# Kernel optimization log

Hardware: AMD Instinct MI355X
Metric: run time of the kernel (lower is better)

## Reference

```python
import jax, jax.numpy as jnp
import numpy as np

DIM = 768
NUM_HEADS = 12
HEAD_DIM = DIM // NUM_HEADS


def setup_inputs() -> dict:
    key = jax.random.key(0)
    k1, k2, k3 = jax.random.split(key, 3)
    B, N, C = 8, 4096, DIM
    x = jax.random.normal(k1, (B, N, C), dtype=jnp.float32)
    # torch nn.Linear weights are (out_features, in_features)
    W_qkv = jax.random.normal(k2, (3 * C, C), dtype=jnp.float32) * 0.02
    b_qkv = jnp.zeros((3 * C,), dtype=jnp.float32)
    W_proj = jax.random.normal(k3, (C, C), dtype=jnp.float32) * 0.02
    b_proj = jnp.zeros((C,), dtype=jnp.float32)
    return {"x": x, "W_qkv": W_qkv, "b_qkv": b_qkv, "W_proj": W_proj, "b_proj": b_proj}


def reference(x, W_qkv, b_qkv, W_proj, b_proj):
    B, N, C = x.shape
    H, D = NUM_HEADS, HEAD_DIM
    # qkv projection -> (3, B, H, N, D)
    qkv = (x @ W_qkv.T + b_qkv).reshape(B, N, 3, H, D).transpose(2, 0, 3, 1, 4)
    q, k, v = qkv[0], qkv[1], qkv[2]
    # feature map: elu(x) + 1 (positive kernel features)
    q = jax.nn.elu(q) + 1.0
    k = jax.nn.elu(k) + 1.0
    # kernelized linear attention: (K^T V) then Q (K^T V)
    kv = jnp.einsum('bhnd,bhnv->bhdv', k, v)          # (B,H,D,D)
    out = jnp.einsum('bhnd,bhdv->bhnv', q, kv)        # (B,H,N,D)
    k_sum = k.sum(axis=2)                             # (B,H,D)
    normalizer = jnp.einsum('bhnd,bhd->bhn', q, k_sum) + 1e-06
    out = out / normalizer[..., None]
    out = out.transpose(0, 2, 1, 3).reshape(B, N, C)
    out = out @ W_proj.T + b_proj
    return out
```

## Files before the change

### kernel.cpp

```cpp
#include <hip/hip_runtime.h>
#include <hip/hip_fp16.h>
#include <math.h>

#define NHEADS 12
#define SEQ 4096
#define BATCH 8

typedef _Float16 half8 __attribute__((ext_vector_type(8)));
typedef float floatx4 __attribute__((ext_vector_type(4)));

__global__ void zero_kernel(float* p, int n) {
  int i = blockIdx.x * 256 + threadIdx.x;
  if (i < n) p[i] = 0.f;
}

__global__ void cast_f2h(const float* __restrict__ in, __half* __restrict__ out, int n) {
  int i = (blockIdx.x * 256 + threadIdx.x) * 4;
  if (i < n) {
    float4 v = *(const float4*)&in[i];
    ushort4 o;
    o.x = __half_as_ushort(__float2half(v.x));
    o.y = __half_as_ushort(__float2half(v.y));
    o.z = __half_as_ushort(__float2half(v.z));
    o.w = __half_as_ushort(__float2half(v.w));
    *(ushort4*)&out[i] = o;
  }
}

__device__ __forceinline__ void gld16(const __half* g, _Float16* dst) {
  __builtin_amdgcn_global_load_lds((const __attribute__((address_space(1))) void*)g,
                                   (__attribute__((address_space(3))) void*)dst, 16, 0, 0);
}

__device__ __forceinline__ int fragoff(int row, int quad) {
  const int mp = row >> 1;
  const int p  = ((row & 1) << 2) | quad;
  return (mp * 8 + (p ^ (mp & 7))) * 8;
}

__device__ __forceinline__ void stage_tile(const __half* __restrict__ gbase, int ldg,
                                           _Float16* lds, int t) {
#pragma unroll
  for (int it = 0; it < 2; ++it) {
    const int s  = it * 256 + t;
    const int mp = s >> 3, ps = s & 7;
    const int p  = ps ^ (mp & 7);
    const int r  = mp * 2 + (p >> 2);
    const int q  = p & 3;
    const __half* g = gbase + (size_t)r * ldg + q * 8;
    _Float16* dst = lds + (s >> 6) * 512;
    gld16(g, dst);
  }
}

__device__ __forceinline__ void write_l64(_Float16* lds, int row, int col, float v) {
  lds[row * 64 + ((((col >> 3) ^ (row & 7))) << 3) + (col & 7)] = (_Float16)v;
}
__device__ __forceinline__ half8 read_l64c(const _Float16* lds, int row, int c) {
  return *(const half8*)(lds + row * 64 + ((c ^ (row & 7)) << 3));
}

__device__ __forceinline__ void barrier_raw() {
  asm volatile("s_barrier" ::: "memory");
}

__global__ __launch_bounds__(512, 2) void hgemm_kv8_kernel(
    const __half* __restrict__ A, const __half* __restrict__ W,
    const float* __restrict__ bias,
    __half* __restrict__ outK, __half* __restrict__ outV)
{
  const int K = 768;
  const int NT = 24;
  extern __shared__ __align__(16) _Float16 sh[];
  const int t    = threadIdx.x;
  const int w    = t >> 6;
  const int l    = t & 63;
  const int quad = l >> 4;
  const int mrow = l & 15;
  const int wm   = w >> 2;
  const int wn   = w & 3;

  const int bid  = blockIdx.x;
  const int xcd  = bid & 7;
  const int ii   = bid >> 3;
  const int mg   = ii / 6;
  const int jj   = ii - mg * 6;
  const int m0   = (xcd * 16 + mg) * 256;
  const int j0   = jj * 256;

  const int mp  = t >> 3;
  const int pp  = (t & 7) ^ (mp & 7);
  const int rsw = mp * 2 + (pp >> 2);
  const int qsw = (pp & 3) * 8;
  const __half* gA0 = A + (size_t)(m0 + rsw) * K + qsw;
  const __half* gA1 = gA0 + (size_t)128 * K;
  const __half* gW0 = W + (size_t)(768 + j0 + rsw) * K + qsw;
  const __half* gW1 = gW0 + (size_t)128 * K;
  const int ld = (t >> 6) * 512;

  int aoff[8], boff[4];
#pragma unroll
  for (int i = 0; i < 8; ++i)
    aoff[i] = wm * 4096 + fragoff(i * 16 + mrow, quad);
#pragma unroll
  for (int j = 0; j < 4; ++j) {
    const int C = wn * 64 + j * 16 + mrow;
    boff[j] = 8192 + (C >> 7) * 4096 + fragoff(C & 127, quad);
  }

  floatx4 acc[8][4];
#pragma unroll
  for (int i = 0; i < 8; ++i)
#pragma unroll
    for (int j = 0; j < 4; ++j) acc[i][j] = (floatx4){0.f, 0.f, 0.f, 0.f};

#pragma unroll
  for (int kt = 0; kt < 3; ++kt) {
    _Float16* db = sh + kt * 16384;
    const int kg = kt * 32;
    gld16(gA0 + kg, db + ld);
    gld16(gA1 + kg, db + 4096 + ld);
    gld16(gW0 + kg, db + 8192 + ld);
    gld16(gW1 + kg, db + 12288 + ld);
  }
  asm volatile("s_waitcnt vmcnt(8)" ::: "memory");
  barrier_raw();

#pragma unroll 4
  for (int kt = 0; kt < NT; ++kt) {
    const _Float16* bb = sh + (kt & 3) * 16384;
    const bool st = (kt + 3 < NT);
    _Float16* db = sh + ((kt + 3) & 3) * 16384;
    const int kg = (kt + 3) * 32;
    half8 af[4], bf[4];

#pragma unroll
    for (int j = 0; j < 4; ++j) bf[j] = *(const half8*)(bb + boff[j]);
#pragma unroll
    for (int i = 0; i < 4; ++i) af[i] = *(const half8*)(bb + aoff[i]);
    if (st) {
      gld16(gA0 + kg, db + ld);
      gld16(gA1 + kg, db + 4096 + ld);
    }
    barrier_raw();
    __builtin_amdgcn_s_setprio(1);
#pragma unroll
    for (int i = 0; i < 4; ++i)
#pragma unroll
      for (int j = 0; j < 4; ++j)
        acc[i][j] = __builtin_amdgcn_mfma_f32_16x16x32_f16(af[i], bf[j], acc[i][j], 0, 0, 0);
    __builtin_amdgcn_s_setprio(0);

#pragma unroll
    for (int i = 0; i < 4; ++i) af[i] = *(const half8*)(bb + aoff[i + 4]);
    if (st) {
      gld16(gW0 + kg, db + 8192 + ld);
      gld16(gW1 + kg, db + 12288 + ld);
    }
    barrier_raw();
    __builtin_amdgcn_s_setprio(1);
#pragma unroll
    for (int i = 0; i < 4; ++i)
#pragma unroll
      for (int j = 0; j < 4; ++j)
        acc[i + 4][j] = __builtin_amdgcn_mfma_f32_16x16x32_f16(af[i], bf[j], acc[i + 4][j], 0, 0, 0);
    __builtin_amdgcn_s_setprio(0);

    if (kt < NT - 3)       asm volatile("s_waitcnt vmcnt(8)" ::: "memory");
    else if (kt == NT - 3) asm volatile("s_waitcnt vmcnt(4)" ::: "memory");
    else if (kt == NT - 2) asm volatile("s_waitcnt vmcnt(0)" ::: "memory");
    barrier_raw();
  }

  const int col0 = 768 + j0 + wn * 64;
  const int t3   = col0 / 768;
  const int h    = (col0 - t3 * 768) >> 6;
  __half* dst    = (t3 == 1) ? outK : outV;
  const int m0w  = m0 + wm * 128;
  const int b_   = m0w >> 12;
  const int n0w  = m0w & 4095;
  _Float16* scr  = sh + w * 4096;
  const size_t gbT = (size_t)(b_ * NHEADS + h) * 64 * 4096;

#pragma unroll
  for (int hf = 0; hf < 2; ++hf) {
#pragma unroll
    for (int j = 0; j < 4; ++j) {
      const int col = j * 16 + mrow;
      const float bsv = bias[col0 + col];
#pragma unroll
      for (int ii2 = 0; ii2 < 4; ++ii2)
#pragma unroll
        for (int r = 0; r < 4; ++r) {
          const int row = ii2 * 16 + quad * 4 + r;
          float val = acc[hf * 4 + ii2][j][r] + bsv;
          if (t3 == 1) val = (val > 0.f) ? (val + 1.f) : expf(val);
          write_l64(scr, col, row, val);
        }
    }
    barrier_raw();
#pragma unroll
    for (int it = 0; it < 8; ++it) {
      const int dd = it * 8 + (l >> 3);
      const int c  = l & 7;
      half8 vv = read_l64c(scr, dd, c);
      *(half8*)((_Float16*)dst + gbT + (size_t)dd * 4096 + n0w + hf * 64 + c * 8) = vv;
    }
    barrier_raw();
  }
}

__global__ __launch_bounds__(256, 3) void hgemm_proj_kernel(
    const __half* __restrict__ A, const __half* __restrict__ W,
    const float* __restrict__ bias, float* __restrict__ outF)
{
  const int K = 768;
  const int NT = 24;
  __shared__ __align__(16) _Float16 sh[3 * 8192];
  const int t    = threadIdx.x;
  const int w    = t >> 6;
  const int l    = t & 63;
  const int quad = l >> 4;
  const int mrow = l & 15;
  const int wr   = (w >> 1) * 64;
  const int wc   = (w & 1) * 64;

  const int bid  = blockIdx.x;
  const int xcd  = bid & 7;
  const int ii   = bid >> 3;
  const int mg   = ii / 6;
  const int jj   = ii - mg * 6;
  const int m0   = (xcd * 32 + mg) * 128;
  const int j0   = jj * 128;

  const int s1  = 256 + t;
  const int mpa = t >> 3,  ppa = (t & 7) ^ (mpa & 7);
  const int ra  = mpa * 2 + (ppa >> 2), qa = (ppa & 3) * 8;
  const int mpb = s1 >> 3, ppb = (s1 & 7) ^ (mpb & 7);
  const int rb  = mpb * 2 + (ppb >> 2), qb = (ppb & 3) * 8;
  const int lda_ = (t >> 6) * 512;
  const int ldb_ = (s1 >> 6) * 512;
  const __half* gA_0 = A + (size_t)(m0 + ra) * K + qa;
  const __half* gA_1 = A + (size_t)(m0 + rb) * K + qb;
  const __half* gB_0 = W + (size_t)(j0 + ra) * K + qa;
  const __half* gB_1 = W + (size_t)(j0 + rb) * K + qb;

  int aoff[4], boff[4];
#pragma unroll
  for (int i = 0; i < 4; ++i) aoff[i] = fragoff(wr + i * 16 + mrow, quad);
#pragma unroll
  for (int j = 0; j < 4; ++j) boff[j] = 4096 + fragoff(wc + j * 16 + mrow, quad);

  floatx4 acc[4][4];
#pragma unroll
  for (int i = 0; i < 4; ++i)
#pragma unroll
    for (int j = 0; j < 4; ++j) acc[i][j] = (floatx4){0.f, 0.f, 0.f, 0.f};

  gld16(gA_0, sh + lda_);           gld16(gA_1, sh + ldb_);
  gld16(gB_0, sh + 4096 + lda_);    gld16(gB_1, sh + 4096 + ldb_);
  gld16(gA_0 + 32, sh + 8192 + lda_);        gld16(gA_1 + 32, sh + 8192 + ldb_);
  gld16(gB_0 + 32, sh + 12288 + lda_);       gld16(gB_1 + 32, sh + 12288 + ldb_);
  asm volatile("s_waitcnt vmcnt(4)" ::: "memory");
  barrier_raw();

  int cur = 0, nxt = 2;
#pragma unroll 3
  for (int kt = 0; kt < NT; ++kt) {
    const _Float16* bb = sh + cur * 8192;
    _Float16* db = sh + nxt * 8192;
    const bool st = (kt + 2 < NT);
    const int kg = (kt + 2) * 32;

    if (st) {
      gld16(gA_0 + kg, db + lda_);        gld16(gA_1 + kg, db + ldb_);
      gld16(gB_0 + kg, db + 4096 + lda_); gld16(gB_1 + kg, db + 4096 + ldb_);
    }
    half8 af[4], bf[4];
#pragma unroll
    for (int i = 0; i < 4; ++i) af[i] = *(const half8*)(bb + aoff[i]);
#pragma unroll
    for (int j = 0; j < 4; ++j) bf[j] = *(const half8*)(bb + boff[j]);
#pragma unroll
    for (int i = 0; i < 4; ++i)
#pragma unroll
      for (int j = 0; j < 4; ++j)
        acc[i][j] = __builtin_amdgcn_mfma_f32_16x16x32_f16(af[i], bf[j], acc[i][j], 0, 0, 0);

    if (kt < NT - 2)       asm volatile("s_waitcnt vmcnt(4)" ::: "memory");
    else if (kt == NT - 2) asm volatile("s_waitcnt vmcnt(0)" ::: "memory");
    barrier_raw();
    cur = (cur + 1) % 3;
    nxt = (nxt + 1) % 3;
  }

#pragma unroll
  for (int j = 0; j < 4; ++j) {
    const int col = j0 + wc + j * 16 + mrow;
    const float bsv = bias[col];
#pragma unroll
    for (int i = 0; i < 4; ++i)
#pragma unroll
      for (int r = 0; r < 4; ++r) {
        const int m = m0 + wr + i * 16 + quad * 4 + r;
        outF[(size_t)m * 768 + col] = acc[i][j][r] + bsv;
      }
  }
}

__global__ __launch_bounds__(256) void kv_mfma_kernel(
    const __half* __restrict__ kT, const __half* __restrict__ vT,
    float* __restrict__ kv, float* __restrict__ ksum)
{
  extern __shared__ float red[];
  float* ksr = red + 4 * 4096;
  const int bh = blockIdx.x;
  const int sp = blockIdx.y;
  const int t  = threadIdx.x;
  const int w  = t >> 6;
  const int l  = t & 63;
  const int quad = l >> 4;
  const int mrow = l & 15;
  const size_t base = (size_t)bh * 64 * 4096;
  const int n0 = sp * 1024 + w * 256;

  floatx4 acc[4][4];
  floatx4 ks[4];
#pragma unroll
  for (int i = 0; i < 4; ++i) {
    ks[i] = (floatx4){0.f, 0.f, 0.f, 0.f};
#pragma unroll
    for (int j = 0; j < 4; ++j) acc[i][j] = (floatx4){0.f, 0.f, 0.f, 0.f};
  }
  half8 ones;
#pragma unroll
  for (int e = 0; e < 8; ++e) ones[e] = (_Float16)1.0f;

  const __half* pk[4];
  const __half* pv[4];
#pragma unroll
  for (int i = 0; i < 4; ++i) {
    pk[i] = kT + base + (size_t)(i * 16 + mrow) * 4096 + n0 + quad * 8;
    pv[i] = vT + base + (size_t)(i * 16 + mrow) * 4096 + n0 + quad * 8;
  }

#pragma unroll
  for (int nn = 0; nn < 256; nn += 32) {
    half8 af[4], bf[4];
#pragma unroll
    for (int i = 0; i < 4; ++i) af[i] = *(const half8*)(pk[i] + nn);
#pragma unroll
    for (int j = 0; j < 4; ++j) bf[j] = *(const half8*)(pv[j] + nn);
#pragma unroll
    for (int i = 0; i < 4; ++i)
#pragma unroll
      for (int j = 0; j < 4; ++j)
        acc[i][j] = __builtin_amdgcn_mfma_f32_16x16x32_f16(af[i], bf[j], acc[i][j], 0, 0, 0);
#pragma unroll
    for (int i = 0; i < 4; ++i)
      ks[i] = __builtin_amdgcn_mfma_f32_16x16x32_f16(af[i], ones, ks[i], 0, 0, 0);
  }

  float* rw = red + w * 4096;
#pragma unroll
  for (int i = 0; i < 4; ++i)
#pragma unroll
    for (int j = 0; j < 4; ++j)
#pragma unroll
      for (int r = 0; r < 4; ++r)
        rw[(i * 16 + quad * 4 + r) * 64 + j * 16 + mrow] = acc[i][j][r];
  if (mrow == 0) {
#pragma unroll
    for (int i = 0; i < 4; ++i)
#pragma unroll
      for (int r = 0; r < 4; ++r)
        ksr[w * 64 + i * 16 + quad * 4 + r] = ks[i][r];
  }
  __syncthreads();
#pragma unroll
  for (int ii = 0; ii < 16; ++ii) {
    const int idx = ii * 256 + t;
    const float s = red[idx] + red[4096 + idx] + red[8192 + idx] + red[12288 + idx];
    atomicAdd(&kv[(size_t)bh * 4096 + idx], s);
  }
  if (t < 64)
    atomicAdd(&ksum[(size_t)bh * 64 + t], ksr[t] + ksr[64 + t] + ksr[128 + t] + ksr[192 + t]);
}

__global__ __launch_bounds__(512, 2) void qattn_kernel(
    const __half* __restrict__ A, const __half* __restrict__ W,
    const float* __restrict__ bias,
    const float* __restrict__ kvg, const float* __restrict__ ksumg,
    __half* __restrict__ att)
{
  const int K = 768;
  const int NT = 24;
  extern __shared__ __align__(16) _Float16 sh[];
  __shared__ float norms[512];
  __shared__ float ksums[128];
  const int t    = threadIdx.x;
  const int w    = t >> 6;
  const int l    = t & 63;
  const int quad = l >> 4;
  const int mrow = l & 15;
  const int wr   = (w >> 1) * 64;
  const int hh   = w & 1;
  const int wc   = hh * 64;

  const int bid = blockIdx.x;
  const int xcd = bid & 7;
  const int ii  = bid >> 3;
  const int mg  = ii / 6;
  const int jj  = ii - mg * 6;
  const int m0  = (xcd * 16 + mg) * 256;
  const int j0  = jj * 128;
  const int b_  = m0 >> 12;
  const int h0  = jj * 2;

  _Float16* kvT0 = sh + 49152;

#pragma unroll
  for (int it = 0; it < 16; ++it) {
    const int gidx = it * 512 + t;
    const int head = gidx >> 12;
    const int r    = gidx & 4095;
    const float val = kvg[(size_t)(b_ * NHEADS + h0 + head) * 4096 + r];
    write_l64(kvT0 + head * 4096, r & 63, r >> 6, val);
  }
  if (t < 128) ksums[t] = ksumg[(size_t)(b_ * NHEADS + h0 + (t >> 6)) * 64 + (t & 63)];

  const int mp  = t >> 3;
  const int pp  = (t & 7) ^ (mp & 7);
  const int rsw = mp * 2 + (pp >> 2);
  const int qsw = (pp & 3) * 8;
  const __half* gA0 = A + (size_t)(m0 + rsw) * K + qsw;
  const __half* gA1 = gA0 + (size_t)128 * K;
  const __half* gB0 = W + (size_t)(j0 + rsw) * K + qsw;
  const int ld = (t >> 6) * 512;

  int aoff[4], boff[4];
#pragma unroll
  for (int i = 0; i < 4; ++i) {
    const int rowi = wr + i * 16 + mrow;
    aoff[i] = (rowi >> 7) * 4096 + fragoff(rowi & 127, quad);
  }
#pragma unroll
  for (int j = 0; j < 4; ++j) boff[j] = 8192 + fragoff(wc + j * 16 + mrow, quad);

  floatx4 acc[4][4];
#pragma unroll
  for (int i = 0; i < 4; ++i)
#pragma unroll
    for (int j = 0; j < 4; ++j) acc[i][j] = (floatx4){0.f, 0.f, 0.f, 0.f};

#pragma unroll
  for (int kt = 0; kt < 3; ++kt) {
    _Float16* db = sh + kt * 12288;
    const int kg = kt * 32;
    gld16(gA0 + kg, db + ld);
    gld16(gA1 + kg, db + 4096 + ld);
    gld16(gB0 + kg, db + 8192 + ld);
  }
  asm volatile("s_waitcnt vmcnt(6)" ::: "memory");
  barrier_raw();

#pragma unroll 4
  for (int kt = 0; kt < NT; ++kt) {
    const _Float16* bb = sh + (kt & 3) * 12288;
    const bool st = (kt + 3 < NT);
    _Float16* db = sh + ((kt + 3) & 3) * 12288;
    const int kg = (kt + 3) * 32;
    half8 af[4], bf[4];

#pragma unroll
    for (int j = 0; j < 4; ++j) bf[j] = *(const half8*)(bb + boff[j]);
#pragma unroll
    for (int i = 0; i < 4; ++i) af[i] = *(const half8*)(bb + aoff[i]);
    if (st) {
      gld16(gA0 + kg, db + ld);
      gld16(gA1 + kg, db + 4096 + ld);
      gld16(gB0 + kg, db + 8192 + ld);
    }
#pragma unroll
    for (int i = 0; i < 4; ++i)
#pragma unroll
      for (int j = 0; j < 4; ++j)
        acc[i][j] = __builtin_amdgcn_mfma_f32_16x16x32_f16(af[i], bf[j], acc[i][j], 0, 0, 0);

    if (kt < NT - 3)       asm volatile("s_waitcnt vmcnt(6)" ::: "memory");
    else if (kt == NT - 3) asm volatile("s_waitcnt vmcnt(3)" ::: "memory");
    else if (kt == NT - 2) asm volatile("s_waitcnt vmcnt(0)" ::: "memory");
    barrier_raw();
  }

  _Float16* qtile = sh + w * 4096;

#pragma unroll
  for (int j = 0; j < 4; ++j) {
    const int col = j * 16 + mrow;
    const float bsv = bias[j0 + wc + col];
#pragma unroll
    for (int i = 0; i < 4; ++i)
#pragma unroll
      for (int r = 0; r < 4; ++r) {
        const int row = i * 16 + quad * 4 + r;
        float val = acc[i][j][r] + bsv;
        val = (val > 0.f) ? (val + 1.f) : expf(val);
        write_l64(qtile, row, col, val);
      }
  }
  asm volatile("s_waitcnt lgkmcnt(0)" ::: "memory");
  __builtin_amdgcn_sched_barrier(0);

  {
    float nrm = 0.f;
#pragma unroll
    for (int c = 0; c < 8; ++c) {
      half8 qv = read_l64c(qtile, l, c);
#pragma unroll
      for (int e = 0; e < 8; ++e) nrm += (float)qv[e] * ksums[hh * 64 + c * 8 + e];
    }
    norms[w * 64 + l] = 1.f / (nrm + 1e-6f);
  }

  const _Float16* kvT = kvT0 + hh * 4096;
  floatx4 oacc[4][4];
#pragma unroll
  for (int i = 0; i < 4; ++i)
#pragma unroll
    for (int j = 0; j < 4; ++j) oacc[i][j] = (floatx4){0.f, 0.f, 0.f, 0.f};
#pragma unroll
  for (int ks = 0; ks < 2; ++ks) {
    half8 af2[4], bf2[4];
#pragma unroll
    for (int i = 0; i < 4; ++i) af2[i] = read_l64c(qtile, i * 16 + mrow, ks * 4 + quad);
#pragma unroll
    for (int j = 0; j < 4; ++j) bf2[j] = read_l64c(kvT, j * 16 + mrow, ks * 4 + quad);
#pragma unroll
    for (int i = 0; i < 4; ++i)
#pragma unroll
      for (int j = 0; j < 4; ++j)
        oacc[i][j] = __builtin_amdgcn_mfma_f32_16x16x32_f16(af2[i], bf2[j], oacc[i][j], 0, 0, 0);
  }
  asm volatile("s_waitcnt lgkmcnt(0)" ::: "memory");
  __builtin_amdgcn_sched_barrier(0);

#pragma unroll
  for (int i = 0; i < 4; ++i)
#pragma unroll
    for (int r = 0; r < 4; ++r) {
      const int row = i * 16 + quad * 4 + r;
      const float rn = norms[w * 64 + row];
#pragma unroll
      for (int j = 0; j < 4; ++j)
        write_l64(qtile, row, j * 16 + mrow, oacc[i][j][r] * rn);
    }
  asm volatile("s_waitcnt lgkmcnt(0)" ::: "memory");
  __builtin_amdgcn_sched_barrier(0);

  const int n0w = (m0 & 4095) + wr;
  const size_t abase = (size_t)(b_ * SEQ + n0w) * 768 + (h0 + hh) * 64;
#pragma unroll
  for (int it = 0; it < 8; ++it) {
    const int row = it * 8 + (l >> 3);
    const int c   = l & 7;
    half8 vv = read_l64c(qtile, row, c);
    *(half8*)((_Float16*)att + abase + (size_t)row * 768 + c * 8) = vv;
  }
}

extern "C" void kernel_launch(void* const* d_in, const int* in_sizes, int n_in,
                              void* d_out, int out_size, void* d_ws, size_t ws_size,
                              hipStream_t stream)
{
  const float* x     = (const float*)d_in[0];
  const float* Wqkv  = (const float*)d_in[1];
  const float* bqkv  = (const float*)d_in[2];
  const float* Wproj = (const float*)d_in[3];
  const float* bproj = (const float*)d_in[4];
  float* out = (float*)d_out;

  const size_t SZ = (size_t)BATCH * NHEADS * SEQ * 64;
  __half* xh  = (__half*)d_ws;
  __half* Wqh = xh + SZ;
  __half* Wph = Wqh + (size_t)2304 * 768;
  __half* R3  = Wph + (size_t)768 * 768;
  __half* R4  = R3 + SZ;
  float*  kvb = (float*)(R4 + SZ);
  float*  ksum = kvb + 96 * 64 * 64;

  static bool attr_set = false;
  if (!attr_set) {
    hipFuncSetAttribute((const void*)hgemm_kv8_kernel,
                        hipFuncAttributeMaxDynamicSharedMemorySize, 131072);
    hipFuncSetAttribute((const void*)kv_mfma_kernel,
                        hipFuncAttributeMaxDynamicSharedMemorySize, 66560);
    hipFuncSetAttribute((const void*)qattn_kernel,
                        hipFuncAttributeMaxDynamicSharedMemorySize, 114688);
    attr_set = true;
  }

  zero_kernel<<<1560, 256, 0, stream>>>(kvb, 96 * 64 * 64 + 96 * 64);

  cast_f2h<<<(int)(SZ / 1024), 256, 0, stream>>>(x, xh, (int)SZ);
  cast_f2h<<<(2304 * 768) / 1024, 256, 0, stream>>>(Wqkv, Wqh, 2304 * 768);
  cast_f2h<<<(768 * 768) / 1024, 256, 0, stream>>>(Wproj, Wph, 768 * 768);

  hgemm_kv8_kernel<<<768, 512, 131072, stream>>>(xh, Wqh, bqkv, R3, R4);

  kv_mfma_kernel<<<dim3(96, 4), 256, 66560, stream>>>(R3, R4, kvb, ksum);

  qattn_kernel<<<768, 512, 114688, stream>>>(
      xh, Wqh, bqkv, kvb, ksum, R3);

  hgemm_proj_kernel<<<1536, 256, 0, stream>>>(R3, Wph, bproj, out);
}
```

Baseline: 442.6 us.

## Restructure KV GEMM pipeline into double-buffered 64-wide K stages

Replaces the 4-deep ring of 32-wide K tiles in the K/V projection GEMM with a double buffer of 64-wide K stages (two 32-wide sub-tiles each), so the loop runs 12 iterations instead of 24. Waits and barriers are placed at sub-tile boundaries, with prefetch of the next stage interleaved between MFMA groups. The aim is to cut per-iteration loop and barrier overhead while keeping loads in flight. In exchange it adds extra barriers per sub-tile and has a shallower prefetch distance, which may expose memory latency. It also removes an unused staging helper.

```diff
diff --git a/kernel.cpp b/kernel.cpp
--- a/kernel.cpp
+++ b/kernel.cpp
@@ -38,21 +38,6 @@
   return (mp * 8 + (p ^ (mp & 7))) * 8;
 }
 
-__device__ __forceinline__ void stage_tile(const __half* __restrict__ gbase, int ldg,
-                                           _Float16* lds, int t) {
-#pragma unroll
-  for (int it = 0; it < 2; ++it) {
-    const int s  = it * 256 + t;
-    const int mp = s >> 3, ps = s & 7;
-    const int p  = ps ^ (mp & 7);
-    const int r  = mp * 2 + (p >> 2);
-    const int q  = p & 3;
-    const __half* g = gbase + (size_t)r * ldg + q * 8;
-    _Float16* dst = lds + (s >> 6) * 512;
-    gld16(g, dst);
-  }
-}
-
 __device__ __forceinline__ void write_l64(_Float16* lds, int row, int col, float v) {
   lds[row * 64 + ((((col >> 3) ^ (row & 7))) << 3) + (col & 7)] = (_Float16)v;
 }
@@ -70,7 +55,7 @@
     __half* __restrict__ outK, __half* __restrict__ outV)
 {
   const int K = 768;
-  const int NT = 24;
+  const int NKT = 12;
   extern __shared__ __align__(16) _Float16 sh[];
   const int t    = threadIdx.x;
   const int w    = t >> 6;
@@ -98,50 +83,51 @@
   const __half* gW1 = gW0 + (size_t)128 * K;
   const int ld = (t >> 6) * 512;
 
-  int aoff[8], boff[4];
+  int aoff0[8], aoff1[8], boff0[4], boff1[4];
+#pragma unroll
+  for (int i = 0; i < 8; ++i) {
+    const int fo = fragoff(i * 16 + mrow, quad);
+    aoff0[i] = wm * 4096 + fo;
+    aoff1[i] = (2 + wm) * 4096 + fo;
+  }
+#pragma unroll
+  for (int j = 0; j < 4; ++j) {
+    const int C  = wn * 64 + j * 16 + mrow;
+    const int fo = fragoff(C & 127, quad);
+    boff0[j] = 16384 + (C >> 7) * 4096 + fo;
+    boff1[j] = 16384 + (2 + (C >> 7)) * 4096 + fo;
+  }
+
+  floatx4 acc[8][4];
 #pragma unroll
   for (int i = 0; i < 8; ++i)
-    aoff[i] = wm * 4096 + fragoff(i * 16 + mrow, quad);
-#pragma unroll
-  for (int j = 0; j < 4; ++j) {
-    const int C = wn * 64 + j * 16 + mrow;
-    boff[j] = 8192 + (C >> 7) * 4096 + fragoff(C & 127, quad);
-  }
-
-  floatx4 acc[8][4];
-#pragma unroll
-  for (int i = 0; i < 8; ++i)
 #pragma unroll
     for (int j = 0; j < 4; ++j) acc[i][j] = (floatx4){0.f, 0.f, 0.f, 0.f};
 
-#pragma unroll
-  for (int kt = 0; kt < 3; ++kt) {
-    _Float16* db = sh + kt * 16384;
-    const int kg = kt * 32;
-    gld16(gA0 + kg, db + ld);
-    gld16(gA1 + kg, db + 4096 + ld);
-    gld16(gW0 + kg, db + 8192 + ld);
-    gld16(gW1 + kg, db + 12288 + ld);
-  }
-  asm volatile("s_waitcnt vmcnt(8)" ::: "memory");
-  barrier_raw();
-
-#pragma unroll 4
-  for (int kt = 0; kt < NT; ++kt) {
-    const _Float16* bb = sh + (kt & 3) * 16384;
-    const bool st = (kt + 3 < NT);
-    _Float16* db = sh + ((kt + 3) & 3) * 16384;
-    const int kg = (kt + 3) * 32;
+  gld16(gA0,      sh + ld);
+  gld16(gA1,      sh + 4096  + ld);
+  gld16(gW0,      sh + 16384 + ld);
+  gld16(gW1,      sh + 20480 + ld);
+  gld16(gA0 + 32, sh + 8192  + ld);
+  gld16(gA1 + 32, sh + 12288 + ld);
+  gld16(gW0 + 32, sh + 24576 + ld);
+  gld16(gW1 + 32, sh + 28672 + ld);
+
+#pragma unroll 2
+  for (int kt = 0; kt < NKT; ++kt) {
+    const _Float16* bb = sh + (kt & 1) * 32768;
+    _Float16* db = sh + ((kt + 1) & 1) * 32768;
+    const bool st = (kt + 1 < NKT);
+    const int kg = (kt + 1) * 64;
     half8 af[4], bf[4];
 
-#pragma unroll
-    for (int j = 0; j < 4; ++j) bf[j] = *(const half8*)(bb + boff[j]);
-#pragma unroll
-    for (int i = 0; i < 4; ++i) af[i] = *(const half8*)(bb + aoff[i]);
-    if (st) {
-      gld16(gA0 + kg, db + ld);
-      gld16(gA1 + kg, db + 4096 + ld);
-    }
+    asm volatile("s_waitcnt vmcnt(4)" ::: "memory");
+    barrier_raw();
+#pragma unroll
+    for (int j = 0; j < 4; ++j) bf[j] = *(const half8*)(bb + boff0[j]);
+#pragma unroll
+    for (int i = 0; i < 4; ++i) af[i] = *(const half8*)(bb + aoff0[i]);
+    if (st) { gld16(gA0 + kg, db + ld); gld16(gA1 + kg, db + 4096 + ld); }
     barrier_raw();
     __builtin_amdgcn_s_setprio(1);
 #pragma unroll
@@ -151,12 +137,10 @@
         acc[i][j] = __builtin_amdgcn_mfma_f32_16x16x32_f16(af[i], bf[j], acc[i][j], 0, 0, 0);
     __builtin_amdgcn_s_setprio(0);
 
-#pragma unroll
-    for (int i = 0; i < 4; ++i) af[i] = *(const half8*)(bb + aoff[i + 4]);
-    if (st) {
-      gld16(gW0 + kg, db + 8192 + ld);
-      gld16(gW1 + kg, db + 12288 + ld);
-    }
+    barrier_raw();
+#pragma unroll
+    for (int i = 0; i < 4; ++i) af[i] = *(const half8*)(bb + aoff0[i + 4]);
+    if (st) { gld16(gW0 + kg, db + 16384 + ld); gld16(gW1 + kg, db + 20480 + ld); }
     barrier_raw();
     __builtin_amdgcn_s_setprio(1);
 #pragma unroll
@@ -166,11 +150,37 @@
         acc[i + 4][j] = __builtin_amdgcn_mfma_f32_16x16x32_f16(af[i], bf[j], acc[i + 4][j], 0, 0, 0);
     __builtin_amdgcn_s_setprio(0);
 
-    if (kt < NT - 3)       asm volatile("s_waitcnt vmcnt(8)" ::: "memory");
-    else if (kt == NT - 3) asm volatile("s_waitcnt vmcnt(4)" ::: "memory");
-    else if (kt == NT - 2) asm volatile("s_waitcnt vmcnt(0)" ::: "memory");
-    barrier_raw();
-  }
+    if (st) asm volatile("s_waitcnt vmcnt(4)" ::: "memory");
+    else    asm volatile("s_waitcnt vmcnt(0)" ::: "memory");
+    barrier_raw();
+#pragma unroll
+    for (int j = 0; j < 4; ++j) bf[j] = *(const half8*)(bb + boff1[j]);
+#pragma unroll
+    for (int i = 0; i < 4; ++i) af[i] = *(const half8*)(bb + aoff1[i]);
+    if (st) { gld16(gA0 + kg + 32, db + 8192 + ld); gld16(gA1 + kg + 32, db + 12288 + ld); }
+    barrier_raw();
+    __builtin_amdgcn_s_setprio(1);
+#pragma unroll
+    for (int i = 0; i < 4; ++i)
+#pragma unroll
+      for (int j = 0; j < 4; ++j)
+        acc[i][j] = __builtin_amdgcn_mfma_f32_16x16x32_f16(af[i], bf[j], acc[i][j], 0, 0, 0);
+    __builtin_amdgcn_s_setprio(0);
+
+    barrier_raw();
+#pragma unroll
+    for (int i = 0; i < 4; ++i) af[i] = *(const half8*)(bb + aoff1[i + 4]);
+    if (st) { gld16(gW0 + kg + 32, db + 24576 + ld); gld16(gW1 + kg + 32, db + 28672 + ld); }
+    barrier_raw();
+    __builtin_amdgcn_s_setprio(1);
+#pragma unroll
+    for (int i = 0; i < 4; ++i)
+#pragma unroll
+      for (int j = 0; j < 4; ++j)
+        acc[i + 4][j] = __builtin_amdgcn_mfma_f32_16x16x32_f16(af[i], bf[j], acc[i + 4][j], 0, 0, 0);
+    __builtin_amdgcn_s_setprio(0);
+  }
+  barrier_raw();
 
   const int col0 = 768 + j0 + wn * 64;
   const int t3   = col0 / 768;
```

After: 430.9 us. -2.6%, faster.
